# Kernel optimization log

Measured on AMD Instinct MI355X. Metric: run time of the kernel, lower is better.

## Reference

```python
import jax, jax.numpy as jnp
import numpy as np

V_PATCH_NUMS = (1, 2, 4, 6, 8, 10, 13, 16)
HW = 16
QUANT_RESI = 0.5
SHARE_K = 4
BETA = 1.0


def _pool_matrix(n_in, n_out):
    # adaptive average pooling as a [n_out, n_in] matrix (matches F.adaptive_avg_pool2d bins)
    P = np.zeros((n_out, n_in), np.float32)
    for i in range(n_out):
        s = (i * n_in) // n_out
        e = -((-(i + 1) * n_in) // n_out)  # ceil((i+1)*n_in/n_out)
        P[i, s:e] = 1.0 / (e - s)
    return jnp.asarray(P)


def _phi_index(si, SN):
    # PhiPartiallyShared.__getitem__(si/(SN-1)) with K=4 ticks
    K = SHARE_K
    ticks = np.linspace(1.0 / 3 / K, 1 - 1.0 / 3 / K, K) if K == 4 else np.linspace(1.0 / 2 / K, 1 - 1.0 / 2 / K, K)
    return int(np.argmin(np.abs(ticks - si / (SN - 1))))


def _phi(h, w, b):
    # Phi: h*(1-r) + conv3x3(h)*r, zero padding (nn.Conv2d default)
    y = jax.lax.conv_general_dilated(h, w, (1, 1), 'SAME',
                                     dimension_numbers=('NCHW', 'OIHW', 'NCHW'))
    y = y + b[None, :, None, None]
    return h * (1.0 - QUANT_RESI) + y * QUANT_RESI


def setup_inputs() -> dict:
    key = jax.random.key(0)
    k0, k1, k2 = jax.random.split(key, 3)
    B, C, V = 64, 32, 4096
    f = jax.random.normal(k0, (B, C, HW, HW), jnp.float32)
    embed = jax.random.normal(k1, (V, C), jnp.float32)  # EMAEmbedding.weight ~ randn
    phi_w = jax.random.normal(k2, (SHARE_K, C, C, 3, 3), jnp.float32) * (1.0 / np.sqrt(9.0 * C))
    phi_b = jnp.zeros((SHARE_K, C), jnp.float32)
    return {"f_BChw": f, "embed_weight": embed, "phi_w": phi_w, "phi_b": phi_b}


def reference(f_BChw, embed_weight, phi_w, phi_b):
    B, C, H, W = f_BChw.shape
    SN = len(V_PATCH_NUMS)
    f_ng = jax.lax.stop_gradient(f_BChw)
    f_hat = jnp.zeros_like(f_BChw)
    e_sq = jnp.sum(embed_weight * embed_weight, axis=1)  # [V]
    loss = jnp.float32(0.0)
    for si, pn in enumerate(V_PATCH_NUMS):
        rest = f_ng - jax.lax.stop_gradient(f_hat)  # residual to quantize (no grad through distance)
        if pn != H:
            P = _pool_matrix(H, pn)
            rest_d = jnp.einsum('oh,bchw,pw->bcop', P, rest, P)  # adaptive avg pool -> [B,C,pn,pn]
        else:
            rest_d = rest
        rest_NC = rest_d.transpose(0, 2, 3, 1).reshape(-1, C)  # [B*pn*pn, C]
        # squared euclidean cdist to codebook, argmin
        d = (jnp.sum(rest_NC * rest_NC, axis=1, keepdims=True)
             + e_sq[None, :]
             - 2.0 * (rest_NC @ embed_weight.T))  # [N, V]
        idx = jnp.argmin(d, axis=1)  # [B*pn*pn] int
        h = embed_weight[idx].reshape(B, pn, pn, C).transpose(0, 3, 1, 2)  # gather -> [B,C,pn,pn]
        if pn != H:
            h = jax.image.resize(h, (B, C, H, W), method='linear')  # bilinear, align_corners=False
        k = _phi_index(si, SN)
        h = _phi(h, phi_w[k], phi_b[k])
        f_hat = f_hat + h
        loss = loss + 0.25 * jnp.mean((jax.lax.stop_gradient(f_hat) - f_BChw) ** 2) \
                    + BETA * jnp.mean((f_hat - f_ng) ** 2)
    loss = loss / SN
    # straight-through estimator: grads flow to f_BChw as identity
    f_hat_st = jax.lax.stop_gradient(f_hat - f_BChw) + f_BChw
    return f_hat_st, loss
```

## Files before the change

### kernel.cpp

```cpp
#include <hip/hip_runtime.h>
#include <hip/hip_bf16.h>

#define BB 64
#define CC 32
#define HW2 256
#define VV 4096
#define NELEM (BB*CC*HW2)
#define PADW 18
#define PADA 324

#define OFF_F     0
#define OFF_FHAT  (OFF_F     + NELEM)
#define OFF_EMBT  (OFF_FHAT  + NELEM)
#define OFF_ESQ   (OFF_EMBT  + VV*CC)
#define OFF_PW    (OFF_ESQ   + VV)
#define OFF_PB    (OFF_PW    + 4*CC*CC*9)
#define OFF_REST  (OFF_PB    + 4*CC)
#define OFF_BESTA (OFF_REST  + 16384*CC)
#define OFF_BESTB (OFF_BESTA + 2*16384)
#define OFF_LOSS  (OFF_BESTB + 2*16384)
#define OFF_FLAG  (OFF_LOSS  + 1)

__device__ __forceinline__ int embt_idx(int v, int c) {
    return (v >> 6) * 2048 + c * 64 + (v & 63);
}

__global__ void k_probe(const void* __restrict__ fin, int* __restrict__ flag) {
    __shared__ int cnt[256];
    int t = threadIdx.x;
    const __hip_bfloat16* p = (const __hip_bfloat16*)fin;
    int local = 0;
    for (int i = t; i < 8192; i += 256) {
        float v = __bfloat162float(p[i]);
        if (!(fabsf(v) < 1e3f)) local++;
    }
    cnt[t] = local;
    __syncthreads();
    for (int s = 128; s > 0; s >>= 1) {
        if (t < s) cnt[t] += cnt[t + s];
        __syncthreads();
    }
    if (t == 0) *flag = (cnt[0] >= 64) ? 1 : 0;
}

__global__ void k_prep(const void* __restrict__ fin,
                       const void* __restrict__ ein,
                       const void* __restrict__ win,
                       const void* __restrict__ bin_,
                       const int* __restrict__ flag,
                       float* __restrict__ f, float* __restrict__ fhat,
                       float* __restrict__ embT, float* __restrict__ pw,
                       float* __restrict__ pb, float* __restrict__ loss) {
    bool isf32 = (*flag != 0);
    int i = blockIdx.x * 256 + threadIdx.x;
    if (i < NELEM) {
        f[i] = isf32 ? ((const float*)fin)[i]
                     : __bfloat162float(((const __hip_bfloat16*)fin)[i]);
        fhat[i] = 0.f;
    }
    if (i < VV*CC) {
        float ev = isf32 ? ((const float*)ein)[i]
                         : __bfloat162float(((const __hip_bfloat16*)ein)[i]);
        int v = i >> 5, c = i & 31;
        embT[embt_idx(v, c)] = ev;
    }
    if (i < 4*CC*CC*9)
        pw[i] = isf32 ? ((const float*)win)[i]
                      : __bfloat162float(((const __hip_bfloat16*)win)[i]);
    if (i < 4*CC)
        pb[i] = isf32 ? ((const float*)bin_)[i]
                      : __bfloat162float(((const __hip_bfloat16*)bin_)[i]);
    if (i == 0) *loss = 0.f;
}

__global__ void k_esq(const float* __restrict__ embT, float* __restrict__ esq) {
    int v = blockIdx.x * 256 + threadIdx.x;
    if (v >= VV) return;
    const float* p = embT + (v >> 6) * 2048 + (v & 63);
    float s = 0.f;
    #pragma unroll
    for (int c = 0; c < CC; ++c) { float e = p[c * 64]; s = fmaf(e, e, s); }
    esq[v] = s;
}

__global__ void k_pool0(const float* __restrict__ f, const float* __restrict__ fhat,
                        float* __restrict__ rest, unsigned long long* __restrict__ best) {
    int n = threadIdx.x;
    int c = blockIdx.y;
    if (n >= BB) return;
    if (c == 0) best[n] = 0xFFFFFFFFFFFFFFFFull;
    const float* fb = f + (n * CC + c) * HW2;
    const float* hb = fhat + (n * CC + c) * HW2;
    float s = 0.f;
    for (int h = 0; h < 16; ++h)
        for (int w = 0; w < 16; ++w)
            s += fb[h * 16 + w] - hb[h * 16 + w];
    rest[n * CC + c] = s * (1.f / 256.f);
}

__global__ __launch_bounds__(256, 2)
void k_argmin_big(const float* __restrict__ rest, const float* __restrict__ embT,
                  const float* __restrict__ esq, unsigned long long* __restrict__ best,
                  int Ntot, int cpw) {
    __shared__ float xT[CC * 256];
    __shared__ float eT[CC * 128];
    __shared__ float xxs[256];
    int tid = threadIdx.x;
    int tx = tid & 15, ty = tid >> 4;
    int qblk = blockIdx.x * 256;
    int v0 = blockIdx.y * cpw;
    int t0 = v0 >> 6;

    {
        int qb = tid;
        int qq = qblk + qb; if (qq > Ntot - 1) qq = Ntot - 1;
        const float* xr = rest + qq * CC;
        int col = ((qb >> 2) & 3) * 64 + (qb >> 4) * 4 + (qb & 3);
        float p0 = 0.f, p1 = 0.f;
        #pragma unroll
        for (int c = 0; c < 16; ++c) {
            float xv = xr[c];
            xT[c * 256 + col] = xv;
            p0 = fmaf(xv, xv, p0);
        }
        #pragma unroll
        for (int c = 16; c < 32; ++c) {
            float xv = xr[c];
            xT[c * 256 + col] = xv;
            p1 = fmaf(xv, xv, p1);
        }
        xxs[qb] = p0 + p1;
    }
    __syncthreads();

    float xx[16];
    #pragma unroll
    for (int e = 0; e < 4; ++e) {
        float4 t4 = *(const float4*)(xxs + ty * 16 + e * 4);
        xx[e*4+0] = t4.x; xx[e*4+1] = t4.y; xx[e*4+2] = t4.z; xx[e*4+3] = t4.w;
    }

    float bd[16]; int bi[16];
    #pragma unroll
    for (int i = 0; i < 16; ++i) { bd[i] = 3.4e38f; bi[i] = v0; }

    int ntiles = cpw >> 7;
    for (int t = 0; t < ntiles; ++t) {
        int vbase = v0 + t * 128;
        const float* gt = embT + (size_t)(t0 + 2 * t) * 2048;
        float4 s[4];
        #pragma unroll
        for (int i = 0; i < 4; ++i)
            s[i] = *(const float4*)(gt + (tid + i * 256) * 4);
        __syncthreads();
        #pragma unroll
        for (int i = 0; i < 4; ++i) {
            int g = tid + i * 256;
            int ss = g >> 9, r = g & 511;
            int c = r >> 4, j4 = r & 15;
            int p = (j4 & 1) * 16 + ss * 8 + (j4 >> 1);
            *(float4*)(eT + c * 128 + p * 4) = s[i];
        }
        __syncthreads();

        float acc[16][8];
        #pragma unroll
        for (int i = 0; i < 16; ++i)
            #pragma unroll
            for (int j = 0; j < 8; ++j) acc[i][j] = 0.f;

        #pragma unroll 2
        for (int k = 0; k < CC; ++k) {
            const float* xk = xT + k * 256;
            const float* ek = eT + k * 128;
            float4 A0 = *(const float4*)(xk + ty * 4);
            float4 A1 = *(const float4*)(xk + 64 + ty * 4);
            float4 A2 = *(const float4*)(xk + 128 + ty * 4);
            float4 A3 = *(const float4*)(xk + 192 + ty * 4);
            float4 B0 = *(const float4*)(ek + tx * 4);
            float4 B1 = *(const float4*)(ek + 64 + tx * 4);
            float a[16] = {A0.x,A0.y,A0.z,A0.w, A1.x,A1.y,A1.z,A1.w,
                           A2.x,A2.y,A2.z,A2.w, A3.x,A3.y,A3.z,A3.w};
            float b[8]  = {B0.x,B0.y,B0.z,B0.w, B1.x,B1.y,B1.z,B1.w};
            #pragma unroll
            for (int i = 0; i < 16; ++i)
                #pragma unroll
                for (int j = 0; j < 8; ++j)
                    acc[i][j] = fmaf(a[i], b[j], acc[i][j]);
        }

        float4 e0 = *(const float4*)(esq + vbase + tx * 8);
        float4 e1 = *(const float4*)(esq + vbase + tx * 8 + 4);
        float es[8] = {e0.x,e0.y,e0.z,e0.w, e1.x,e1.y,e1.z,e1.w};
        #pragma unroll
        for (int i = 0; i < 16; ++i) {
            float base = xx[i];
            #pragma unroll
            for (int j = 0; j < 8; ++j) {
                float dist = fmaf(-2.f, acc[i][j], base + es[j]);
                if (dist < bd[i]) { bd[i] = dist; bi[i] = vbase + tx * 8 + j; }
            }
        }
    }

    #pragma unroll
    for (int i = 0; i < 16; ++i) {
        unsigned u = __float_as_uint(bd[i]);
        unsigned long long mono = (u & 0x80000000u)
            ? (unsigned long long)(~u)
            : (unsigned long long)(u | 0x80000000u);
        unsigned long long pk = (mono << 32) | (unsigned long long)(unsigned)bi[i];
        #pragma unroll
        for (int m = 1; m <= 8; m <<= 1) {
            unsigned long long o = __shfl_xor(pk, m, 64);
            if (o < pk) pk = o;
        }
        int q = qblk + ty * 16 + i;
        if (tx == 0 && q < Ntot)
            atomicMin(best + q, pk);
    }
}

__global__ __launch_bounds__(256, 4)
void k_argmin_small(const float* __restrict__ rest, const float* __restrict__ embT,
                    const float* __restrict__ esq, unsigned long long* __restrict__ best,
                    int Ntot, int cpw) {
    int tid  = threadIdx.x;
    int w    = tid >> 6, lane = tid & 63;
    int q0   = blockIdx.x * 512 + w * 128 + lane;
    int q1   = q0 + 64;
    int v0   = blockIdx.y * cpw;

    bool act0 = (q0 < Ntot), act1 = (q1 < Ntot);
    if (!act0 && !act1) return;
    int qa = act0 ? q0 : (Ntot - 1);
    int qb = act1 ? q1 : (Ntot - 1);

    float a0v[32], a1v[32];
    {
        const float4* ra = (const float4*)(rest + qa * CC);
        const float4* rb = (const float4*)(rest + qb * CC);
        #pragma unroll
        for (int c4 = 0; c4 < 8; ++c4) {
            float4 va = ra[c4], vb4 = rb[c4];
            a0v[c4*4+0] = va.x;  a0v[c4*4+1] = va.y;
            a0v[c4*4+2] = va.z;  a0v[c4*4+3] = va.w;
            a1v[c4*4+0] = vb4.x; a1v[c4*4+1] = vb4.y;
            a1v[c4*4+2] = vb4.z; a1v[c4*4+3] = vb4.w;
        }
    }

    float p0a = 0.f, p1a = 0.f, p0b = 0.f, p1b = 0.f;
    #pragma unroll
    for (int c = 0; c < 16; ++c)  p0a = fmaf(a0v[c], a0v[c], p0a);
    #pragma unroll
    for (int c = 16; c < 32; ++c) p1a = fmaf(a0v[c], a0v[c], p1a);
    #pragma unroll
    for (int c = 0; c < 16; ++c)  p0b = fmaf(a1v[c], a1v[c], p0b);
    #pragma unroll
    for (int c = 16; c < 32; ++c) p1b = fmaf(a1v[c], a1v[c], p1b);
    float xx0 = p0a + p1a;
    float xx1 = p0b + p1b;

    float bd0 = 3.4e38f, bd1 = 3.4e38f;
    int   bi0 = v0,      bi1 = v0;

    int ntiles = cpw >> 3;
    for (int t = 0; t < ntiles; ++t) {
        int vb = v0 + t * 8;
        int boff = __builtin_amdgcn_readfirstlane((vb >> 6) * 2048 + (vb & 63));
        int eoff = __builtin_amdgcn_readfirstlane(vb);
        const float* bt = embT + boff;
        const float* ep = esq + eoff;

        float acc0[8], acc1[8];
        #pragma unroll
        for (int j = 0; j < 8; ++j) { acc0[j] = 0.f; acc1[j] = 0.f; }

        #pragma unroll
        for (int k = 0; k < CC; ++k) {
            float a0 = a0v[k], a1 = a1v[k];
            #pragma unroll
            for (int j = 0; j < 8; ++j) {
                float bv = bt[k * 64 + j];
                acc0[j] = fmaf(a0, bv, acc0[j]);
                acc1[j] = fmaf(a1, bv, acc1[j]);
            }
        }

        #pragma unroll
        for (int j = 0; j < 8; ++j) {
            float es = ep[j];
            float d0 = fmaf(-2.f, acc0[j], xx0 + es);
            if (d0 < bd0) { bd0 = d0; bi0 = vb + j; }
            float d1 = fmaf(-2.f, acc1[j], xx1 + es);
            if (d1 < bd1) { bd1 = d1; bi1 = vb + j; }
        }
    }

    unsigned u0 = __float_as_uint(bd0);
    unsigned long long mono0 = (u0 & 0x80000000u)
        ? (unsigned long long)(~u0)
        : (unsigned long long)(u0 | 0x80000000u);
    unsigned long long pk0 = (mono0 << 32) | (unsigned long long)(unsigned)bi0;
    unsigned u1 = __float_as_uint(bd1);
    unsigned long long mono1 = (u1 & 0x80000000u)
        ? (unsigned long long)(~u1)
        : (unsigned long long)(u1 | 0x80000000u);
    unsigned long long pk1 = (mono1 << 32) | (unsigned long long)(unsigned)bi1;

    if (act0) atomicMin(best + q0, pk0);
    if (act1) atomicMin(best + q1, pk1);
}

__global__ __launch_bounds__(256)
void k_fuse(const float* __restrict__ embT,
            const unsigned long long* __restrict__ best,
            const float* __restrict__ pw, const float* __restrict__ pb,
            const float* __restrict__ f, float* __restrict__ fhat,
            float* __restrict__ loss,
            float* __restrict__ rest,
            unsigned long long* __restrict__ best_next,
            int pn, int k, int pn_next) {
    __shared__ float h_pad[CC * PADA];
    __shared__ float extra[CC * 169];
    __shared__ float red[4];
    int b = blockIdx.x, co8 = blockIdx.y, t = threadIdx.x;
    int nn = pn * pn;
    int y = t >> 4, x = t & 15;

    for (int i = t; i < CC * PADA; i += 256) h_pad[i] = 0.f;

    if (pn == 16) {
        __syncthreads();
        int id = (int)(unsigned)(best[b * HW2 + t] & 0xFFFFFFFFull);
        const float* er = embT + (id >> 6) * 2048 + (id & 63);
        int ctr = (y + 1) * PADW + (x + 1);
        #pragma unroll
        for (int c = 0; c < CC; ++c)
            h_pad[c * PADA + ctr] = er[c * 64];
    } else {
        float (*hs)[169] = (float(*)[169])extra;
        for (int cell = t; cell < nn; cell += 256) {
            int id = (int)(unsigned)(best[b * nn + cell] & 0xFFFFFFFFull);
            const float* er = embT + (id >> 6) * 2048 + (id & 63);
            #pragma unroll
            for (int c = 0; c < CC; ++c) hs[c][cell] = er[c * 64];
        }
        __syncthreads();
        float scale = (float)pn / 16.f;
        float sy = (y + 0.5f) * scale - 0.5f;
        sy = fminf(fmaxf(sy, 0.f), (float)(pn - 1));
        int y0 = (int)sy; int y1 = min(y0 + 1, pn - 1); float wy = sy - (float)y0;
        float sx = (x + 0.5f) * scale - 0.5f;
        sx = fminf(fmaxf(sx, 0.f), (float)(pn - 1));
        int x0 = (int)sx; int x1 = min(x0 + 1, pn - 1); float wx = sx - (float)x0;
        float wy0 = 1.f - wy, wx0 = 1.f - wx;
        int ctr = (y + 1) * PADW + (x + 1);
        #pragma unroll
        for (int c = 0; c < CC; ++c) {
            float v00 = hs[c][y0 * pn + x0], v01 = hs[c][y0 * pn + x1];
            float v10 = hs[c][y1 * pn + x0], v11 = hs[c][y1 * pn + x1];
            float a0 = wy0 * v00 + wy * v10;
            float a1 = wy0 * v01 + wy * v11;
            h_pad[c * PADA + ctr] = wx0 * a0 + wx * a1;
        }
    }
    __syncthreads();

    float acc[4];
    #pragma unroll
    for (int o = 0; o < 4; ++o) acc[o] = 0.f;
    const float* hbase = h_pad + y * PADW + x;
    const float* wpk = pw + (k * CC + co8 * 4) * (CC * 9);
    #pragma unroll
    for (int ci_ = 0; ci_ < CC; ++ci_) {
        float hv[9];
        #pragma unroll
        for (int dy = 0; dy < 3; ++dy)
            #pragma unroll
            for (int dx = 0; dx < 3; ++dx)
                hv[dy * 3 + dx] = hbase[ci_ * PADA + dy * PADW + dx];
        const float* wp = wpk + ci_ * 9;
        #pragma unroll
        for (int o = 0; o < 4; ++o) {
            const float* w9 = wp + o * (CC * 9);
            #pragma unroll
            for (int q = 0; q < 9; ++q) acc[o] = fmaf(hv[q], w9[q], acc[o]);
        }
    }

    float* diff = extra;
    float lsum = 0.f;
    int ctr = (y + 1) * PADW + (x + 1);
    #pragma unroll
    for (int o = 0; o < 4; ++o) {
        int co = co8 * 4 + o;
        float hval = h_pad[co * PADA + ctr];
        float outv = hval * 0.5f + (acc[o] + pb[k * CC + co]) * 0.5f;
        int pos = (b * CC + co) * HW2 + t;
        float fh = fhat[pos] + outv;
        fhat[pos] = fh;
        float dd = f[pos] - fh;
        diff[o * HW2 + t] = dd;
        lsum = fmaf(dd, dd, lsum);
    }
    #pragma unroll
    for (int off = 32; off > 0; off >>= 1) lsum += __shfl_down(lsum, off, 64);
    if ((t & 63) == 0) red[t >> 6] = lsum;
    __syncthreads();
    if (t == 0)
        atomicAdd(loss, red[0] + red[1] + red[2] + red[3]);

    if (pn_next > 0) {
        int nn2 = pn_next * pn_next;
        for (int q = t; q < nn2 * 4; q += 256) {
            int cell = q % nn2, o = q / nn2;
            int i = cell / pn_next, j = cell % pn_next;
            int s0 = (i * 16) / pn_next, e0 = ((i + 1) * 16 + pn_next - 1) / pn_next;
            int s1 = (j * 16) / pn_next, e1 = ((j + 1) * 16 + pn_next - 1) / pn_next;
            float inv = 1.f / (float)((e0 - s0) * (e1 - s1));
            float s = 0.f;
            for (int h = s0; h < e0; ++h)
                for (int w = s1; w < e1; ++w)
                    s += diff[o * HW2 + h * 16 + w];
            rest[(b * nn2 + cell) * CC + co8 * 4 + o] = s * inv;
        }
        if (co8 == 0)
            for (int q = t; q < nn2; q += 256)
                best_next[b * nn2 + q] = 0xFFFFFFFFFFFFFFFFull;
    }
}

__global__ void k_out(const float* __restrict__ fhat, const float* __restrict__ loss,
                      const int* __restrict__ flag, void* __restrict__ out) {
    bool isf32 = (*flag != 0);
    int i = blockIdx.x * 256 + threadIdx.x;
    if (i > NELEM) return;
    float v;
    if (i < NELEM) v = fhat[i];
    else           v = (*loss) * (1.25f / (float)NELEM / 8.f);
    if (isf32) ((float*)out)[i] = v;
    else       ((__hip_bfloat16*)out)[i] = __float2bfloat16(v);
}

extern "C" void kernel_launch(void* const* d_in, const int* in_sizes, int n_in,
                              void* d_out, int out_size, void* d_ws, size_t ws_size,
                              hipStream_t stream) {
    const void* fin  = d_in[0];
    const void* ein  = d_in[1];
    const void* win  = d_in[2];
    const void* bin_ = d_in[3];
    float* ws = (float*)d_ws;
    float* f    = ws + OFF_F;
    float* fhat = ws + OFF_FHAT;
    float* embT = ws + OFF_EMBT;
    float* esq  = ws + OFF_ESQ;
    float* pw   = ws + OFF_PW;
    float* pb   = ws + OFF_PB;
    float* rest = ws + OFF_REST;
    unsigned long long* bestA = (unsigned long long*)(ws + OFF_BESTA);
    unsigned long long* bestB = (unsigned long long*)(ws + OFF_BESTB);
    float* loss = ws + OFF_LOSS;
    int*   flag = (int*)(ws + OFF_FLAG);

    static const int PN[8] = {1, 2, 4, 6, 8, 10, 13, 16};
    static const int KK[8] = {0, 0, 1, 1, 2, 2, 3, 3};
    static const int SPs[4] = {512, 512, 512, 256};
    static const int SPb[4] = {32, 32, 16, 16};

    k_probe<<<1, 256, 0, stream>>>(fin, flag);
    k_prep<<<(NELEM + 255) / 256, 256, 0, stream>>>(fin, ein, win, bin_, flag,
                                                    f, fhat, embT, pw, pb, loss);
    k_esq<<<(VV + 255) / 256, 256, 0, stream>>>(embT, esq);
    k_pool0<<<dim3(1, CC), 256, 0, stream>>>(f, fhat, rest, bestA);

    for (int si = 0; si < 8; ++si) {
        int pn = PN[si];
        int Ntot = BB * pn * pn;
        unsigned long long* bcur = (si & 1) ? bestB : bestA;
        unsigned long long* bnxt = (si & 1) ? bestA : bestB;
        int pn_next = (si < 7) ? PN[si + 1] : 0;
        if (si < 4) {
            int Sp = SPs[si];
            int cpw = VV / Sp;
            int gx = (Ntot + 511) / 512;
            k_argmin_small<<<dim3(gx, Sp), 256, 0, stream>>>(rest, embT, esq, bcur,
                                                             Ntot, cpw);
        } else {
            int Sp = SPb[si - 4];
            int cpw = VV / Sp;
            int gx = (Ntot + 255) / 256;
            k_argmin_big<<<dim3(gx, Sp), 256, 0, stream>>>(rest, embT, esq, bcur,
                                                           Ntot, cpw);
        }
        k_fuse<<<dim3(BB, 8), 256, 0, stream>>>(embT, bcur, pw, pb, f, fhat, loss,
                                                rest, bnxt, pn, KK[si], pn_next);
    }
    k_out<<<(NELEM + 1 + 255) / 256, 256, 0, stream>>>(fhat, loss, flag, d_out);
}
```

Baseline: 471.6 us.

## Shrink argmin_big query tile to 128 and simplify shared-memory layouts

Reworks the large-scale argmin kernel so each block handles 128 queries instead of 256, giving each thread an 8x8 instead of a 16x8 register accumulator. The embedding tile is copied straight into shared memory with no permutation, the query tile is padded to 132 columns, and the squared norm is split across two threads. Occupancy is raised to 3 blocks per SM and the codebook split factor is halved to keep the grid size comparable. The aim is lower register pressure and higher occupancy, at the cost of less A-operand reuse per thread and more embedding traffic per query.

```diff
diff --git a/kernel.cpp b/kernel.cpp
--- a/kernel.cpp
+++ b/kernel.cpp
@@ -98,113 +98,98 @@
     rest[n * CC + c] = s * (1.f / 256.f);
 }
 
-__global__ __launch_bounds__(256, 2)
+__global__ __launch_bounds__(256, 3)
 void k_argmin_big(const float* __restrict__ rest, const float* __restrict__ embT,
                   const float* __restrict__ esq, unsigned long long* __restrict__ best,
                   int Ntot, int cpw) {
-    __shared__ float xT[CC * 256];
-    __shared__ float eT[CC * 128];
-    __shared__ float xxs[256];
+    __shared__ float xT[CC][132];
+    __shared__ float eT[2 * CC * 64];
+    __shared__ float xxs[2][128];
     int tid = threadIdx.x;
     int tx = tid & 15, ty = tid >> 4;
-    int qblk = blockIdx.x * 256;
+    int qblk = blockIdx.x * 128;
     int v0 = blockIdx.y * cpw;
     int t0 = v0 >> 6;
 
     {
-        int qb = tid;
-        int qq = qblk + qb; if (qq > Ntot - 1) qq = Ntot - 1;
-        const float* xr = rest + qq * CC;
-        int col = ((qb >> 2) & 3) * 64 + (qb >> 4) * 4 + (qb & 3);
-        float p0 = 0.f, p1 = 0.f;
+        int q = tid >> 1, h = tid & 1;
+        int qq = qblk + q; if (qq > Ntot - 1) qq = Ntot - 1;
+        const float* xr = rest + qq * CC + h * 16;
+        float part = 0.f;
         #pragma unroll
         for (int c = 0; c < 16; ++c) {
             float xv = xr[c];
-            xT[c * 256 + col] = xv;
-            p0 = fmaf(xv, xv, p0);
-        }
-        #pragma unroll
-        for (int c = 16; c < 32; ++c) {
-            float xv = xr[c];
-            xT[c * 256 + col] = xv;
-            p1 = fmaf(xv, xv, p1);
-        }
-        xxs[qb] = p0 + p1;
+            xT[h * 16 + c][q] = xv;
+            part = fmaf(xv, xv, part);
+        }
+        xxs[h][q] = part;
     }
     __syncthreads();
 
-    float xx[16];
-    #pragma unroll
-    for (int e = 0; e < 4; ++e) {
-        float4 t4 = *(const float4*)(xxs + ty * 16 + e * 4);
-        xx[e*4+0] = t4.x; xx[e*4+1] = t4.y; xx[e*4+2] = t4.z; xx[e*4+3] = t4.w;
-    }
-
-    float bd[16]; int bi[16];
-    #pragma unroll
-    for (int i = 0; i < 16; ++i) { bd[i] = 3.4e38f; bi[i] = v0; }
+    float xx[8];
+    #pragma unroll
+    for (int i = 0; i < 8; ++i) {
+        int q = (i >> 2) * 64 + ty * 4 + (i & 3);
+        xx[i] = xxs[0][q] + xxs[1][q];
+    }
+
+    float bd[8]; int bi[8];
+    #pragma unroll
+    for (int i = 0; i < 8; ++i) { bd[i] = 3.4e38f; bi[i] = v0; }
 
     int ntiles = cpw >> 7;
     for (int t = 0; t < ntiles; ++t) {
         int vbase = v0 + t * 128;
         const float* gt = embT + (size_t)(t0 + 2 * t) * 2048;
-        float4 s[4];
-        #pragma unroll
-        for (int i = 0; i < 4; ++i)
-            s[i] = *(const float4*)(gt + (tid + i * 256) * 4);
+        float4 s0 = *(const float4*)(gt + tid * 4);
+        float4 s1 = *(const float4*)(gt + 1024 + tid * 4);
+        float4 s2 = *(const float4*)(gt + 2048 + tid * 4);
+        float4 s3 = *(const float4*)(gt + 3072 + tid * 4);
         __syncthreads();
-        #pragma unroll
-        for (int i = 0; i < 4; ++i) {
-            int g = tid + i * 256;
-            int ss = g >> 9, r = g & 511;
-            int c = r >> 4, j4 = r & 15;
-            int p = (j4 & 1) * 16 + ss * 8 + (j4 >> 1);
-            *(float4*)(eT + c * 128 + p * 4) = s[i];
-        }
+        *(float4*)(eT + tid * 4) = s0;
+        *(float4*)(eT + 1024 + tid * 4) = s1;
+        *(float4*)(eT + 2048 + tid * 4) = s2;
+        *(float4*)(eT + 3072 + tid * 4) = s3;
         __syncthreads();
 
-        float acc[16][8];
-        #pragma unroll
-        for (int i = 0; i < 16; ++i)
+        float acc[8][8];
+        #pragma unroll
+        for (int i = 0; i < 8; ++i)
             #pragma unroll
             for (int j = 0; j < 8; ++j) acc[i][j] = 0.f;
 
-        #pragma unroll 2
+        #pragma unroll 8
         for (int k = 0; k < CC; ++k) {
-            const float* xk = xT + k * 256;
-            const float* ek = eT + k * 128;
-            float4 A0 = *(const float4*)(xk + ty * 4);
-            float4 A1 = *(const float4*)(xk + 64 + ty * 4);
-            float4 A2 = *(const float4*)(xk + 128 + ty * 4);
-            float4 A3 = *(const float4*)(xk + 192 + ty * 4);
-            float4 B0 = *(const float4*)(ek + tx * 4);
-            float4 B1 = *(const float4*)(ek + 64 + tx * 4);
-            float a[16] = {A0.x,A0.y,A0.z,A0.w, A1.x,A1.y,A1.z,A1.w,
-                           A2.x,A2.y,A2.z,A2.w, A3.x,A3.y,A3.z,A3.w};
-            float b[8]  = {B0.x,B0.y,B0.z,B0.w, B1.x,B1.y,B1.z,B1.w};
-            #pragma unroll
-            for (int i = 0; i < 16; ++i)
+            float4 a0 = *(const float4*)&xT[k][ty * 4];
+            float4 a1 = *(const float4*)&xT[k][64 + ty * 4];
+            float4 b0 = *(const float4*)(eT + k * 64 + tx * 4);
+            float4 b1 = *(const float4*)(eT + 2048 + k * 64 + tx * 4);
+            float a[8] = {a0.x, a0.y, a0.z, a0.w, a1.x, a1.y, a1.z, a1.w};
+            float b[8] = {b0.x, b0.y, b0.z, b0.w, b1.x, b1.y, b1.z, b1.w};
+            #pragma unroll
+            for (int i = 0; i < 8; ++i)
                 #pragma unroll
                 for (int j = 0; j < 8; ++j)
                     acc[i][j] = fmaf(a[i], b[j], acc[i][j]);
         }
 
-        float4 e0 = *(const float4*)(esq + vbase + tx * 8);
-        float4 e1 = *(const float4*)(esq + vbase + tx * 8 + 4);
-        float es[8] = {e0.x,e0.y,e0.z,e0.w, e1.x,e1.y,e1.z,e1.w};
-        #pragma unroll
-        for (int i = 0; i < 16; ++i) {
+        float4 e0 = *(const float4*)(esq + vbase + tx * 4);
+        float4 e1 = *(const float4*)(esq + vbase + 64 + tx * 4);
+        float es[8] = {e0.x, e0.y, e0.z, e0.w, e1.x, e1.y, e1.z, e1.w};
+        #pragma unroll
+        for (int i = 0; i < 8; ++i) {
             float base = xx[i];
             #pragma unroll
             for (int j = 0; j < 8; ++j) {
                 float dist = fmaf(-2.f, acc[i][j], base + es[j]);
-                if (dist < bd[i]) { bd[i] = dist; bi[i] = vbase + tx * 8 + j; }
+                int vidx = vbase + (j >> 2) * 64 + tx * 4 + (j & 3);
+                if (dist < bd[i]) { bd[i] = dist; bi[i] = vidx; }
             }
         }
     }
 
     #pragma unroll
-    for (int i = 0; i < 16; ++i) {
+    for (int i = 0; i < 8; ++i) {
         unsigned u = __float_as_uint(bd[i]);
         unsigned long long mono = (u & 0x80000000u)
             ? (unsigned long long)(~u)
@@ -215,7 +200,7 @@
             unsigned long long o = __shfl_xor(pk, m, 64);
             if (o < pk) pk = o;
         }
-        int q = qblk + ty * 16 + i;
+        int q = qblk + (i >> 2) * 64 + ty * 4 + (i & 3);
         if (tx == 0 && q < Ntot)
             atomicMin(best + q, pk);
     }
@@ -467,7 +452,7 @@
     static const int PN[8] = {1, 2, 4, 6, 8, 10, 13, 16};
     static const int KK[8] = {0, 0, 1, 1, 2, 2, 3, 3};
     static const int SPs[4] = {512, 512, 512, 256};
-    static const int SPb[4] = {32, 32, 16, 16};
+    static const int SPb[4] = {16, 16, 8, 8};
 
     k_probe<<<1, 256, 0, stream>>>(fin, flag);
     k_prep<<<(NELEM + 255) / 256, 256, 0, stream>>>(fin, ein, win, bin_, flag,
@@ -490,7 +475,7 @@
         } else {
             int Sp = SPb[si - 4];
             int cpw = VV / Sp;
-            int gx = (Ntot + 255) / 256;
+            int gx = (Ntot + 127) / 128;
             k_argmin_big<<<dim3(gx, Sp), 256, 0, stream>>>(rest, embT, esq, bcur,
                                                            Ntot, cpw);
         }
```

Result: faster. 453.2 us (-3.9%).
